# Performance work log

Hardware: AMD Instinct MI355X
Metric: run time of the kernel (lower is better)

Reference implementation:

```python
import jax, jax.numpy as jnp
import numpy as np

BS, EMB, RES = 256, 768, 14
N_MASKS, HID, OUT, N_PROJ = 16, 4096, 256, 4
BN_EPS = 1e-5


def setup_inputs() -> dict:
    key = jax.random.key(0)
    ks = jax.random.split(key, 8)
    x = jax.random.normal(ks[0], (BS, EMB, RES, RES), jnp.float32)
    # binary ROI masks over the 14x14 = 196 patch grid
    masks = (jax.random.uniform(ks[1], (BS, N_MASKS, RES * RES)) < 0.3).astype(jnp.float32)
    projection_idx = jax.random.randint(ks[2], (N_MASKS,), 0, N_PROJ, jnp.int32)
    mask_ids = jax.random.randint(ks[3], (BS, N_MASKS), 0, 100, jnp.int32)
    # stacked params for the N_PROJ MLP projectors
    W1 = jax.random.normal(ks[4], (N_PROJ, EMB, HID), jnp.float32) * 0.02
    b1 = jnp.zeros((N_PROJ, HID), jnp.float32)
    gamma = jnp.ones((N_PROJ, HID), jnp.float32)
    beta = jnp.zeros((N_PROJ, HID), jnp.float32)
    W2 = jax.random.normal(ks[5], (N_PROJ, HID, OUT), jnp.float32) * 0.02
    b2 = jnp.zeros((N_PROJ, OUT), jnp.float32)
    return {"x": x, "masks": masks, "projection_idx": projection_idx,
            "mask_ids": mask_ids, "W1": W1, "b1": b1, "gamma": gamma,
            "beta": beta, "W2": W2, "b2": b2}


def reference(x, masks, projection_idx, mask_ids, W1, b1, gamma, beta, W2, b2):
    bs, emb, hx, hy = x.shape
    # [bs, emb, hx, hy] -> [bs, hw, emb]
    emb_local = jnp.transpose(x, (0, 2, 3, 1)).reshape(bs, hx * hy, emb)
    # mask-normalized pooling:  pooled[b,n,:] = mean of embeddings inside mask n
    area = masks.sum(axis=-1, keepdims=True)
    smpl = masks / jnp.maximum(area, 1.0)
    pooled = smpl @ emb_local                       # [bs, n_masks, emb]
    # dense dispatch: run EVERY projector over all pooled tokens (as original)
    h = jnp.einsum('bne,peh->pbnh', pooled, W1) + b1[:, None, None, :]
    # BatchNorm1d in training mode over flattened (bs*n_masks) batch, per projector
    mu = h.mean(axis=(1, 2), keepdims=True)
    var = jnp.mean(jnp.square(h - mu), axis=(1, 2), keepdims=True)  # biased var
    h = (h - mu) * jax.lax.rsqrt(var + BN_EPS) * gamma[:, None, None, :] + beta[:, None, None, :]
    h = jax.nn.relu(h)
    o = jnp.einsum('pbnh,pho->pbno', h, W2) + b2[:, None, None, :]   # [P, bs, n, out]
    # keep only projector projection_idx[n] for mask-slot n (disjoint selection)
    n_proj = W1.shape[0]
    sel = (projection_idx[None, :] == jnp.arange(n_proj)[:, None]).astype(o.dtype)  # [P, n]
    xs = (o * sel[:, None, :, None]).sum(axis=0)     # [bs, n_masks, out]
    return (xs, mask_ids)
```

## Files before the change

kernel.cpp:

```cpp
#include <hip/hip_runtime.h>
#include <hip/hip_bf16.h>

#define BS 256
#define EMB 768
#define HW 196
#define NMASK 16
#define HID 4096
#define OUT 256
#define NPROJ 4
#define MROWS 4096

typedef __attribute__((ext_vector_type(8))) short bf16x8;
typedef __attribute__((ext_vector_type(4))) float f32x4;
typedef __attribute__((ext_vector_type(8))) unsigned short u16x8;

__device__ inline float bf2f(unsigned short u) {
    unsigned int x = ((unsigned int)u) << 16;
    return __builtin_bit_cast(float, x);
}
__device__ inline short f2bfs(float f) {
    return __builtin_bit_cast(short, __float2bfloat16(f));
}

#define GL16(gptr, lptr)                                                     \
    __builtin_amdgcn_global_load_lds(                                        \
        (const __attribute__((address_space(1))) void*)(gptr),               \
        (__attribute__((address_space(3))) void*)(lptr), 16, 0, 0)

__global__ __launch_bounds__(256) void pool_mfma(
    const float* __restrict__ x, const float* __restrict__ masks,
    __hip_bfloat16* __restrict__ pooledG)
{
    __shared__ __align__(16) short afr[7 * 64 * 8];
    __shared__ float inv[NMASK];
    const int ec = blockIdx.x, b = blockIdx.y, tid = threadIdx.x;
    const float* mb = masks + (size_t)b * NMASK * HW;

    for (int s = tid; s < 7 * 64; s += 256) {
        int m = s & 15, kb = ((s >> 4) & 3) * 8 + (s >> 6) * 32;
        short v[8];
        #pragma unroll
        for (int j = 0; j < 8; ++j) {
            int kk = kb + j;
            v[j] = (kk < HW) ? f2bfs(mb[m * HW + kk]) : (short)0;
        }
        #pragma unroll
        for (int j = 0; j < 8; ++j) afr[s * 8 + j] = v[j];
    }
    if (tid >= 192) {
        int l = tid - 192, m = l >> 2, q = l & 3;
        float a = 0.f;
        for (int hw = q; hw < HW; hw += 4) a += mb[m * HW + hw];
        a += __shfl_xor(a, 1);
        a += __shfl_xor(a, 2);
        if (q == 0) inv[m] = 1.0f / fmaxf(a, 1.0f);
    }
    __syncthreads();

    const int lane = tid & 63, w = tid >> 6;
    const int lc = lane & 15, l4 = lane >> 4;
    const int ebase = ec * 192 + w * 48;
    const bf16x8* afv = (const bf16x8*)afr;
    f32x4 acc[3] = {};

    const float* xb0 = x + ((size_t)b * EMB + ebase + lc) * HW;

    for (int kc = 0; kc < 6; ++kc) {
        bf16x8 af = afv[kc * 64 + lane];
        float4 u[3][2];
        #pragma unroll
        for (int t = 0; t < 3; ++t) {
            const float* xr = xb0 + (size_t)(t * 16) * HW + kc * 32 + l4 * 8;
            u[t][0] = *(const float4*)(xr);
            u[t][1] = *(const float4*)(xr + 4);
        }
        #pragma unroll
        for (int t = 0; t < 3; ++t) {
            bf16x8 bf;
            bf[0] = f2bfs(u[t][0].x); bf[1] = f2bfs(u[t][0].y);
            bf[2] = f2bfs(u[t][0].z); bf[3] = f2bfs(u[t][0].w);
            bf[4] = f2bfs(u[t][1].x); bf[5] = f2bfs(u[t][1].y);
            bf[6] = f2bfs(u[t][1].z); bf[7] = f2bfs(u[t][1].w);
            acc[t] = __builtin_amdgcn_mfma_f32_16x16x32_bf16(af, bf, acc[t], 0, 0, 0);
        }
    }
    {
        bf16x8 af = afv[6 * 64 + lane];
        #pragma unroll
        for (int t = 0; t < 3; ++t) {
            bf16x8 bf = {};
            if (l4 == 0) {
                float4 u0 = *(const float4*)(xb0 + (size_t)(t * 16) * HW + 192);
                bf[0] = f2bfs(u0.x); bf[1] = f2bfs(u0.y);
                bf[2] = f2bfs(u0.z); bf[3] = f2bfs(u0.w);
            }
            acc[t] = __builtin_amdgcn_mfma_f32_16x16x32_bf16(af, bf, acc[t], 0, 0, 0);
        }
    }

    #pragma unroll
    for (int t = 0; t < 3; ++t) {
        int e = ebase + t * 16 + lc;
        #pragma unroll
        for (int j = 0; j < 4; ++j) {
            int m = l4 * 4 + j;
            pooledG[((size_t)m * 256 + b) * EMB + e] =
                __float2bfloat16(acc[t][j] * inv[m]);
        }
    }
}

__global__ __launch_bounds__(256) void transpose_cvt(
    const float* __restrict__ src, __hip_bfloat16* __restrict__ dst, int R, int C)
{
    __shared__ float tile[64][65];
    const float* s = src + (size_t)blockIdx.z * R * C;
    __hip_bfloat16* d = dst + (size_t)blockIdx.z * R * C;
    const int c0 = blockIdx.x * 64, r0 = blockIdx.y * 64, tid = threadIdx.x;
    for (int i = tid; i < 4096; i += 256) {
        int r = i >> 6, c = i & 63;
        tile[r][c] = s[(size_t)(r0 + r) * C + c0 + c];
    }
    __syncthreads();
    for (int i = tid; i < 4096; i += 256) {
        int c = i >> 6, r = i & 63;
        d[(size_t)(c0 + c) * R + r0 + r] = __float2bfloat16(tile[r][c]);
    }
}

__global__ __launch_bounds__(256) void transpose_pg(
    const __hip_bfloat16* __restrict__ src, __hip_bfloat16* __restrict__ dst)
{
    __shared__ __hip_bfloat16 tile[64][65];
    const int c0 = blockIdx.x * 64, r0 = blockIdx.y * 64, tid = threadIdx.x;
    for (int i = tid; i < 4096; i += 256) {
        int r = i >> 6, c = i & 63;
        tile[r][c] = src[(size_t)(r0 + r) * EMB + c0 + c];
    }
    __syncthreads();
    for (int i = tid; i < 4096; i += 256) {
        int c = i >> 6, r = i & 63;
        dst[(size_t)(c0 + c) * MROWS + r0 + r] = tile[r][c];
    }
}

__global__ __launch_bounds__(256) void meanpool(
    const __hip_bfloat16* __restrict__ PT, float* __restrict__ mp)
{
    const int e = blockIdx.x, tid = threadIdx.x;
    const u16x8* p = (const u16x8*)(PT + (size_t)e * MROWS);
    u16x8 v1 = p[tid], v2 = p[tid + 256];
    float s = 0.f;
    #pragma unroll
    for (int j = 0; j < 8; ++j) s += bf2f((unsigned short)v1[j]) + bf2f((unsigned short)v2[j]);
    #pragma unroll
    for (int o = 1; o < 64; o <<= 1) s += __shfl_xor(s, o);
    __shared__ float wsum[4];
    if ((tid & 63) == 0) wsum[tid >> 6] = s;
    __syncthreads();
    if (tid == 0) mp[e] = (wsum[0] + wsum[1] + wsum[2] + wsum[3]) * (1.0f / 4096.0f);
}

__global__ __launch_bounds__(256) void cgemm(
    const __hip_bfloat16* __restrict__ PT, float* __restrict__ Cpart)
{
    __shared__ __align__(16) __hip_bfloat16 As[128 * 32];
    __shared__ __align__(16) __hip_bfloat16 Bs[128 * 32];
    const int tid = threadIdx.x, lane = tid & 63, wid = tid >> 6;
    const int n0 = blockIdx.x * 128, m0 = blockIdx.y * 128, kbase = blockIdx.z * 512;
    float* Cp = Cpart + (size_t)blockIdx.z * EMB * EMB;
    const int wr = wid >> 1, wc = wid & 1;
    const int l4 = lane >> 4, lc = lane & 15;

    f32x4 acc[4][4] = {};
    for (int k0 = kbase; k0 < kbase + 512; k0 += 32) {
        __syncthreads();
        #pragma unroll
        for (int r = 0; r < 2; ++r) {
            int t = r * 256 + tid;
            int row = t >> 2, ko = (t & 3) * 8;
            GL16(PT + (size_t)(m0 + row) * MROWS + k0 + ko, &As[(r * 256 + wid * 64) * 8]);
        }
        #pragma unroll
        for (int r = 0; r < 2; ++r) {
            int t = r * 256 + tid;
            int row = t >> 2, ko = (t & 3) * 8;
            GL16(PT + (size_t)(n0 + row) * MROWS + k0 + ko, &Bs[(r * 256 + wid * 64) * 8]);
        }
        __syncthreads();
        const bf16x8* Av = (const bf16x8*)As;
        const bf16x8* Bv = (const bf16x8*)Bs;
        bf16x8 a[4], b[4];
        #pragma unroll
        for (int m = 0; m < 4; ++m) a[m] = Av[(wr * 64 + m * 16 + lc) * 4 + l4];
        #pragma unroll
        for (int n = 0; n < 4; ++n) b[n] = Bv[(wc * 64 + n * 16 + lc) * 4 + l4];
        #pragma unroll
        for (int m = 0; m < 4; ++m)
            #pragma unroll
            for (int n = 0; n < 4; ++n)
                acc[m][n] = __builtin_amdgcn_mfma_f32_16x16x32_bf16(a[m], b[n], acc[m][n], 0, 0, 0);
    }
    #pragma unroll
    for (int m = 0; m < 4; ++m)
        #pragma unroll
        for (int n = 0; n < 4; ++n)
            #pragma unroll
            for (int j = 0; j < 4; ++j) {
                int row = m0 + wr * 64 + m * 16 + l4 * 4 + j;
                int col = n0 + wc * 64 + n * 16 + lc;
                Cp[(size_t)row * EMB + col] = acc[m][n][j];
            }
}

__global__ __launch_bounds__(256) void cvt_c(
    const float* __restrict__ Cpart, __hip_bfloat16* __restrict__ Cbf)
{
    int i = (blockIdx.x * 256 + threadIdx.x) * 4;
    float sx = 0.f, sy = 0.f, sz = 0.f, sw = 0.f;
    #pragma unroll
    for (int kz = 0; kz < 8; ++kz) {
        float4 v = *(const float4*)(Cpart + (size_t)kz * EMB * EMB + i);
        sx += v.x; sy += v.y; sz += v.z; sw += v.w;
    }
    const float s = 1.0f / 4096.0f;
    Cbf[i + 0] = __float2bfloat16(sx * s);
    Cbf[i + 1] = __float2bfloat16(sy * s);
    Cbf[i + 2] = __float2bfloat16(sz * s);
    Cbf[i + 3] = __float2bfloat16(sw * s);
}

__global__ __launch_bounds__(256) void ugemm(
    const __hip_bfloat16* __restrict__ W1T, const __hip_bfloat16* __restrict__ Cbf,
    const float* __restrict__ mp,
    float* __restrict__ Eh2p, float* __restrict__ Mup)
{
    __shared__ __align__(16) __hip_bfloat16 As[128 * 32];
    __shared__ __align__(16) __hip_bfloat16 Bs[128 * 32];
    const int tid = threadIdx.x, lane = tid & 63, wid = tid >> 6;
    const int n0 = blockIdx.x * 128, m0 = blockIdx.y * 128, p = blockIdx.z;
    const __hip_bfloat16* Ap = W1T + (size_t)p * HID * EMB;
    const int wr = wid >> 1, wc = wid & 1;
    const int l4 = lane >> 4, lc = lane & 15;

    f32x4 acc[4][4] = {};
    for (int k0 = 0; k0 < EMB; k0 += 32) {
        __syncthreads();
        #pragma unroll
        for (int r = 0; r < 2; ++r) {
            int t = r * 256 + tid;
            int row = t >> 2, ko = (t & 3) * 8;
            GL16(Ap + (size_t)(m0 + row) * EMB + k0 + ko, &As[(r * 256 + wid * 64) * 8]);
        }
        #pragma unroll
        for (int r = 0; r < 2; ++r) {
            int t = r * 256 + tid;
            int row = t >> 2, ko = (t & 3) * 8;
            GL16(Cbf + (size_t)(n0 + row) * EMB + k0 + ko, &Bs[(r * 256 + wid * 64) * 8]);
        }
        __syncthreads();
        const bf16x8* Av = (const bf16x8*)As;
        const bf16x8* Bv = (const bf16x8*)Bs;
        bf16x8 a[4], b[4];
        #pragma unroll
        for (int m = 0; m < 4; ++m) a[m] = Av[(wr * 64 + m * 16 + lc) * 4 + l4];
        #pragma unroll
        for (int n = 0; n < 4; ++n) b[n] = Bv[(wc * 64 + n * 16 + lc) * 4 + l4];
        #pragma unroll
        for (int m = 0; m < 4; ++m)
            #pragma unroll
            for (int n = 0; n < 4; ++n)
                acc[m][n] = __builtin_amdgcn_mfma_f32_16x16x32_bf16(a[m], b[n], acc[m][n], 0, 0, 0);
    }

    float mpv[4];
    #pragma unroll
    for (int n = 0; n < 4; ++n) mpv[n] = mp[n0 + wc * 64 + n * 16 + lc];
    #pragma unroll
    for (int m = 0; m < 4; ++m) {
        #pragma unroll
        for (int j = 0; j < 4; ++j) {
            int row = m0 + wr * 64 + m * 16 + l4 * 4 + j;
            const __hip_bfloat16* wrow = Ap + (size_t)row * EMB;
            float e2 = 0.f, mu = 0.f;
            #pragma unroll
            for (int n = 0; n < 4; ++n) {
                int col = n0 + wc * 64 + n * 16 + lc;
                float wv = bf2f(__builtin_bit_cast(unsigned short, wrow[col]));
                e2 += acc[m][n][j] * wv;
                mu += mpv[n] * wv;
            }
            e2 += __shfl_xor(e2, 1); e2 += __shfl_xor(e2, 2);
            e2 += __shfl_xor(e2, 4); e2 += __shfl_xor(e2, 8);
            mu += __shfl_xor(mu, 1); mu += __shfl_xor(mu, 2);
            mu += __shfl_xor(mu, 4); mu += __shfl_xor(mu, 8);
            if (lc == 0) {
                size_t idx = (((size_t)blockIdx.x * 2 + wc) * NPROJ + p) * HID + row;
                Eh2p[idx] = e2;
                Mup [idx] = mu;
            }
        }
    }
}

__global__ __launch_bounds__(256) void finalize(
    const float* __restrict__ Eh2p, const float* __restrict__ Mup,
    const float* __restrict__ gamma, const float* __restrict__ beta,
    float* __restrict__ sbuf, float* __restrict__ tbuf)
{
    int i = blockIdx.x * 256 + threadIdx.x;
    float e2 = 0.f, mu = 0.f;
    #pragma unroll
    for (int bx = 0; bx < 12; ++bx) {
        e2 += Eh2p[bx * (NPROJ * HID) + i];
        mu += Mup [bx * (NPROJ * HID) + i];
    }
    float var = e2 - mu * mu;
    float is  = rsqrtf(fmaxf(var, 0.0f) + 1e-5f);
    float sc  = gamma[i] * is;
    sbuf[i] = sc;
    tbuf[i] = beta[i] - mu * sc;
}

__global__ __launch_bounds__(512, 2) void gemm1_sel(
    const __hip_bfloat16* __restrict__ A, const __hip_bfloat16* __restrict__ W1T,
    const int* __restrict__ proj,
    const float* __restrict__ sbuf, const float* __restrict__ tbuf,
    __hip_bfloat16* __restrict__ hrelu)
{
    __shared__ __align__(16) short LS[2][32768];
    const int tid = threadIdx.x, lane = tid & 63, w = tid >> 6;
    const int wr = w >> 2, wc = w & 3;
    const int lc = lane & 15, l4 = lane >> 4;
    const int n0 = blockIdx.x * 256, m0 = blockIdx.y * 256;
    const int p = proj[blockIdx.y];
    const __hip_bfloat16* Ag = A;
    const __hip_bfloat16* Bg = W1T + (size_t)p * HID * EMB;
    const bf16x8* LSv = (const bf16x8*)LS;

    const int st_row_l = lane >> 3;
    const int st_cs    = lane & 7;
    auto STAGE = [&](int sbf, int t) {
        #pragma unroll
        for (int ab = 0; ab < 2; ++ab) {
            const __hip_bfloat16* g = ab ? Bg : Ag;
            const int rbase = ab ? n0 : m0;
            #pragma unroll
            for (int i = 0; i < 4; ++i) {
                int row = w * 32 + i * 8 + st_row_l;
                int csl = st_cs ^ (row & 7);
                const __hip_bfloat16* src =
                    g + (size_t)(rbase + row) * EMB + t * 64 + csl * 8;
                char* dst = (char*)LS + ab * 32768 + sbf * 65536 + w * 4096 + i * 1024;
                GL16(src, dst);
            }
        }
    };

    f32x4 acc[8][4] = {};

    STAGE(0, 0);
    asm volatile("s_waitcnt vmcnt(0)" ::: "memory");
    __builtin_amdgcn_s_barrier();

    for (int t = 0; t < 12; ++t) {
        const int buf = t & 1;
        if (t + 1 < 12) STAGE(buf ^ 1, t + 1);

        const int vbA = buf * 4096;
        const int vbB = buf * 4096 + 2048;

        bf16x8 bfr[4][2];
        #pragma unroll
        for (int nf = 0; nf < 4; ++nf) {
            int row_b = wc * 64 + nf * 16 + lc;
            #pragma unroll
            for (int ks = 0; ks < 2; ++ks)
                bfr[nf][ks] = LSv[vbB + row_b * 8 + ((ks * 4 + l4) ^ (row_b & 7))];
        }
        #pragma unroll
        for (int q = 0; q < 4; ++q) {
            bf16x8 afr[2][2];
            #pragma unroll
            for (int mf2 = 0; mf2 < 2; ++mf2) {
                int row_a = wr * 128 + (q * 2 + mf2) * 16 + lc;
                #pragma unroll
                for (int ks = 0; ks < 2; ++ks)
                    afr[mf2][ks] = LSv[vbA + row_a * 8 + ((ks * 4 + l4) ^ (row_a & 7))];
            }
            __builtin_amdgcn_s_setprio(1);
            #pragma unroll
            for (int mf2 = 0; mf2 < 2; ++mf2)
                #pragma unroll
                for (int nf = 0; nf < 4; ++nf)
                    #pragma unroll
                    for (int ks = 0; ks < 2; ++ks)
                        acc[q * 2 + mf2][nf] = __builtin_amdgcn_mfma_f32_16x16x32_bf16(
                            afr[mf2][ks], bfr[nf][ks], acc[q * 2 + mf2][nf], 0, 0, 0);
            __builtin_amdgcn_s_setprio(0);
        }

        asm volatile("s_waitcnt vmcnt(0)" ::: "memory");
        __builtin_amdgcn_s_barrier();
    }

    #pragma unroll
    for (int nf = 0; nf < 4; ++nf) {
        int col = n0 + wc * 64 + nf * 16 + lc;
        float s = sbuf[p * HID + col];
        float tt = tbuf[p * HID + col];
        #pragma unroll
        for (int mf = 0; mf < 8; ++mf)
            #pragma unroll
            for (int j = 0; j < 4; ++j) {
                int row = m0 + wr * 128 + mf * 16 + l4 * 4 + j;
                float v = fmaxf(acc[mf][nf][j] * s + tt, 0.0f);
                hrelu[(size_t)row * HID + col] = __float2bfloat16(v);
            }
    }
}

__global__ __launch_bounds__(256) void gemm2(
    const __hip_bfloat16* __restrict__ Hn, const __hip_bfloat16* __restrict__ W2T,
    const int* __restrict__ proj, float* __restrict__ Opart)
{
    __shared__ __align__(16) __hip_bfloat16 As[128 * 32];
    __shared__ __align__(16) __hip_bfloat16 Bs[128 * 32];
    const int tid = threadIdx.x, lane = tid & 63, wid = tid >> 6;
    const int nmask = blockIdx.x;
    const int bc    = blockIdx.y;
    const int ct    = blockIdx.z >> 2, kz = blockIdx.z & 3;
    const int p = proj[nmask];
    const __hip_bfloat16* Ap = Hn + (size_t)(nmask * 256 + bc * 128) * HID;
    const __hip_bfloat16* Bp = W2T + ((size_t)p * OUT + ct * 128) * HID;
    float* Op = Opart + (size_t)kz * MROWS * OUT;
    const int wr = wid >> 1, wc = wid & 1;
    const int l4 = lane >> 4, lc = lane & 15;

    f32x4 acc[4][4] = {};
    for (int k0 = kz * 1024; k0 < kz * 1024 + 1024; k0 += 32) {
        __syncthreads();
        #pragma unroll
        for (int r = 0; r < 2; ++r) {
            int t = r * 256 + tid;
            int row = t >> 2, ko = (t & 3) * 8;
            GL16(Ap + (size_t)row * HID + k0 + ko, &As[(r * 256 + wid * 64) * 8]);
        }
        #pragma unroll
        for (int r = 0; r < 2; ++r) {
            int t = r * 256 + tid;
            int row = t >> 2, ko = (t & 3) * 8;
            GL16(Bp + (size_t)row * HID + k0 + ko, &Bs[(r * 256 + wid * 64) * 8]);
        }
        __syncthreads();
        const bf16x8* Av = (const bf16x8*)As;
        const bf16x8* Bv = (const bf16x8*)Bs;
        bf16x8 a[4], b[4];
        #pragma unroll
        for (int m = 0; m < 4; ++m) a[m] = Av[(wr * 64 + m * 16 + lc) * 4 + l4];
        #pragma unroll
        for (int n = 0; n < 4; ++n) b[n] = Bv[(wc * 64 + n * 16 + lc) * 4 + l4];
        #pragma unroll
        for (int m = 0; m < 4; ++m)
            #pragma unroll
            for (int n = 0; n < 4; ++n)
                acc[m][n] = __builtin_amdgcn_mfma_f32_16x16x32_bf16(a[m], b[n], acc[m][n], 0, 0, 0);
    }

    #pragma unroll
    for (int m = 0; m < 4; ++m)
        #pragma unroll
        for (int n = 0; n < 4; ++n)
            #pragma unroll
            for (int j = 0; j < 4; ++j) {
                int bb = bc * 128 + wr * 64 + m * 16 + l4 * 4 + j;
                int oc = ct * 128 + wc * 64 + n * 16 + lc;
                Op[((size_t)bb * NMASK + nmask) * OUT + oc] = acc[m][n][j];
            }
}

__global__ __launch_bounds__(256) void reduce_out(
    const float* __restrict__ Opart, const float* __restrict__ b2,
    const int* __restrict__ proj, const int* __restrict__ mids,
    float* __restrict__ out)
{
    int i = (blockIdx.x * 256 + threadIdx.x) * 4;
    float sx = 0.f, sy = 0.f, sz = 0.f, sw = 0.f;
    #pragma unroll
    for (int kz = 0; kz < 4; ++kz) {
        float4 v = *(const float4*)(Opart + (size_t)kz * MROWS * OUT + i);
        sx += v.x; sy += v.y; sz += v.z; sw += v.w;
    }
    int nm = (i >> 8) & 15;
    int p  = proj[nm];
    float4 bv = *(const float4*)(b2 + p * OUT + (i & 255));
    float4 r;
    r.x = sx + bv.x; r.y = sy + bv.y; r.z = sz + bv.z; r.w = sw + bv.w;
    *(float4*)(out + i) = r;
    if (blockIdx.x < 16) {
        int t = blockIdx.x * 256 + threadIdx.x;
        out[(size_t)MROWS * OUT + t] = (float)mids[t];
    }
}

extern "C" void kernel_launch(void* const* d_in, const int* in_sizes, int n_in,
                              void* d_out, int out_size, void* d_ws, size_t ws_size,
                              hipStream_t stream)
{
    const float* x     = (const float*)d_in[0];
    const float* masks = (const float*)d_in[1];
    const int*   proj  = (const int*)d_in[2];
    const int*   mids  = (const int*)d_in[3];
    const float* W1    = (const float*)d_in[4];
    const float* gamma = (const float*)d_in[6];
    const float* beta  = (const float*)d_in[7];
    const float* W2    = (const float*)d_in[8];
    const float* b2    = (const float*)d_in[9];
    float* out = (float*)d_out;

    char* ws = (char*)d_ws;
    __hip_bfloat16* pooledG = (__hip_bfloat16*)(ws);
    __hip_bfloat16* W1T     = (__hip_bfloat16*)(ws + 6291456);
    __hip_bfloat16* W2T     = (__hip_bfloat16*)(ws + 31457280);
    float*          mp      = (float*)(ws + 39845888);
    float*          Eh2p    = (float*)(ws + 39848960);
    float*          Mup     = (float*)(ws + 40635392);
    float*          sbuf    = (float*)(ws + 41421824);
    float*          tbuf    = (float*)(ws + 41487360);
    char* R = ws + 41552896;
    __hip_bfloat16* pooledT = (__hip_bfloat16*)(R);
    float*          Cpart   = (float*)(R + 6291456);
    __hip_bfloat16* Cbf     = (__hip_bfloat16*)(R + 25165824);
    __hip_bfloat16* hrelu   = (__hip_bfloat16*)(R);
    float*          Opart   = (float*)(R + 33554432);

    pool_mfma<<<dim3(4, BS), 256, 0, stream>>>(x, masks, pooledG);
    transpose_cvt<<<dim3(HID / 64, EMB / 64, NPROJ), 256, 0, stream>>>(W1, W1T, EMB, HID);
    transpose_cvt<<<dim3(OUT / 64, HID / 64, NPROJ), 256, 0, stream>>>(W2, W2T, HID, OUT);
    transpose_pg<<<dim3(EMB / 64, MROWS / 64), 256, 0, stream>>>(pooledG, pooledT);
    meanpool<<<EMB, 256, 0, stream>>>(pooledT, mp);
    cgemm<<<dim3(6, 6, 8), 256, 0, stream>>>(pooledT, Cpart);
    cvt_c<<<(EMB * EMB) / 1024, 256, 0, stream>>>(Cpart, Cbf);
    ugemm<<<dim3(6, 32, 4), 256, 0, stream>>>(W1T, Cbf, mp, Eh2p, Mup);
    finalize<<<(NPROJ * HID) / 256, 256, 0, stream>>>(Eh2p, Mup, gamma, beta, sbuf, tbuf);
    gemm1_sel<<<dim3(HID / 256, MROWS / 256), 512, 0, stream>>>(pooledG, W1T, proj, sbuf, tbuf, hrelu);
    gemm2<<<dim3(NMASK, 2, 8), 256, 0, stream>>>(hrelu, W2T, proj, Opart);
    reduce_out<<<(MROWS * OUT) / 1024, 256, 0, stream>>>(Opart, b2, proj, mids, out);
}
```

Before: 204.8 us.

## Merge transpose kernels into one launch and triple-buffer gemm1 with half-size K steps

Measured after the change: 202.5 us. Within noise of the previous version (-1.1%).

```diff
diff --git a/kernel.cpp b/kernel.cpp
--- a/kernel.cpp
+++ b/kernel.cpp
@@ -110,37 +110,47 @@
     }
 }
 
-__global__ __launch_bounds__(256) void transpose_cvt(
-    const float* __restrict__ src, __hip_bfloat16* __restrict__ dst, int R, int C)
-{
-    __shared__ float tile[64][65];
-    const float* s = src + (size_t)blockIdx.z * R * C;
-    __hip_bfloat16* d = dst + (size_t)blockIdx.z * R * C;
-    const int c0 = blockIdx.x * 64, r0 = blockIdx.y * 64, tid = threadIdx.x;
-    for (int i = tid; i < 4096; i += 256) {
-        int r = i >> 6, c = i & 63;
-        tile[r][c] = s[(size_t)(r0 + r) * C + c0 + c];
-    }
-    __syncthreads();
-    for (int i = tid; i < 4096; i += 256) {
-        int c = i >> 6, r = i & 63;
-        d[(size_t)(c0 + c) * R + r0 + r] = __float2bfloat16(tile[r][c]);
-    }
-}
-
-__global__ __launch_bounds__(256) void transpose_pg(
-    const __hip_bfloat16* __restrict__ src, __hip_bfloat16* __restrict__ dst)
-{
-    __shared__ __hip_bfloat16 tile[64][65];
-    const int c0 = blockIdx.x * 64, r0 = blockIdx.y * 64, tid = threadIdx.x;
-    for (int i = tid; i < 4096; i += 256) {
-        int r = i >> 6, c = i & 63;
-        tile[r][c] = src[(size_t)(r0 + r) * EMB + c0 + c];
-    }
-    __syncthreads();
-    for (int i = tid; i < 4096; i += 256) {
-        int c = i >> 6, r = i & 63;
-        dst[(size_t)(c0 + c) * MROWS + r0 + r] = tile[r][c];
+__global__ __launch_bounds__(256) void prep(
+    const float* __restrict__ W1, const float* __restrict__ W2,
+    const __hip_bfloat16* __restrict__ pg,
+    __hip_bfloat16* __restrict__ W1T, __hip_bfloat16* __restrict__ W2T,
+    __hip_bfloat16* __restrict__ pgT)
+{
+    __shared__ __align__(16) char sm[64 * 65 * 4];
+    const int bid = blockIdx.x, tid = threadIdx.x;
+    if (bid < 4096) {
+        const float* src; __hip_bfloat16* dst; int R, C, x, y, z;
+        if (bid < 3072) { z = bid / 768; int r = bid % 768; x = r % 64; y = r / 64;
+                          src = W1; dst = W1T; R = EMB; C = HID; }
+        else            { int b2 = bid - 3072; z = b2 / 256; int r = b2 % 256;
+                          x = r % 4; y = r / 4; src = W2; dst = W2T; R = HID; C = OUT; }
+        float (*tile)[65] = (float(*)[65])sm;
+        const float* s = src + (size_t)z * R * C;
+        __hip_bfloat16* d = dst + (size_t)z * R * C;
+        const int c0 = x * 64, r0 = y * 64;
+        for (int i = tid; i < 4096; i += 256) {
+            int r = i >> 6, c = i & 63;
+            tile[r][c] = s[(size_t)(r0 + r) * C + c0 + c];
+        }
+        __syncthreads();
+        for (int i = tid; i < 4096; i += 256) {
+            int c = i >> 6, r = i & 63;
+            d[(size_t)(c0 + c) * R + r0 + r] = __float2bfloat16(tile[r][c]);
+        }
+    } else {
+        const int b3 = bid - 4096;
+        const int x = b3 % 12, y = b3 / 12;
+        __hip_bfloat16 (*tile)[65] = (__hip_bfloat16(*)[65])sm;
+        const int c0 = x * 64, r0 = y * 64;
+        for (int i = tid; i < 4096; i += 256) {
+            int r = i >> 6, c = i & 63;
+            tile[r][c] = pg[(size_t)(r0 + r) * EMB + c0 + c];
+        }
+        __syncthreads();
+        for (int i = tid; i < 4096; i += 256) {
+            int c = i >> 6, r = i & 63;
+            pgT[(size_t)(c0 + c) * MROWS + r0 + r] = tile[r][c];
+        }
     }
 }
 
@@ -328,7 +338,7 @@
     const float* __restrict__ sbuf, const float* __restrict__ tbuf,
     __hip_bfloat16* __restrict__ hrelu)
 {
-    __shared__ __align__(16) short LS[2][32768];
+    __shared__ __align__(16) short LS[3 * 16384];
     const int tid = threadIdx.x, lane = tid & 63, w = tid >> 6;
     const int wr = w >> 2, wc = w & 3;
     const int lc = lane & 15, l4 = lane >> 4;
@@ -338,70 +348,66 @@
     const __hip_bfloat16* Bg = W1T + (size_t)p * HID * EMB;
     const bf16x8* LSv = (const bf16x8*)LS;
 
-    const int st_row_l = lane >> 3;
-    const int st_cs    = lane & 7;
-    auto STAGE = [&](int sbf, int t) {
+    auto STAGE = [&](int t) {
+        const int sb = (t % 3) * 32768;
         #pragma unroll
         for (int ab = 0; ab < 2; ++ab) {
             const __hip_bfloat16* g = ab ? Bg : Ag;
             const int rbase = ab ? n0 : m0;
             #pragma unroll
-            for (int i = 0; i < 4; ++i) {
-                int row = w * 32 + i * 8 + st_row_l;
-                int csl = st_cs ^ (row & 7);
+            for (int i = 0; i < 2; ++i) {
+                int c = (w * 2 + i) * 64 + lane;
+                int row = c >> 2, ps = c & 3;
+                int ls = ps ^ (row & 3);
                 const __hip_bfloat16* src =
-                    g + (size_t)(rbase + row) * EMB + t * 64 + csl * 8;
-                char* dst = (char*)LS + ab * 32768 + sbf * 65536 + w * 4096 + i * 1024;
-                GL16(src, dst);
+                    g + (size_t)(rbase + row) * EMB + t * 32 + ls * 8;
+                GL16(src, (char*)LS + sb + ab * 16384 + (w * 2 + i) * 1024);
             }
         }
     };
 
     f32x4 acc[8][4] = {};
 
-    STAGE(0, 0);
-    asm volatile("s_waitcnt vmcnt(0)" ::: "memory");
+    STAGE(0);
+    STAGE(1);
+    asm volatile("s_waitcnt vmcnt(4)" ::: "memory");
     __builtin_amdgcn_s_barrier();
 
-    for (int t = 0; t < 12; ++t) {
-        const int buf = t & 1;
-        if (t + 1 < 12) STAGE(buf ^ 1, t + 1);
-
-        const int vbA = buf * 4096;
-        const int vbB = buf * 4096 + 2048;
-
-        bf16x8 bfr[4][2];
+    for (int t = 0; t < 24; ++t) {
+        if (t + 2 < 24) STAGE(t + 2);
+        const int vb = (t % 3) * 2048;
+
+        bf16x8 bfr[4];
         #pragma unroll
         for (int nf = 0; nf < 4; ++nf) {
-            int row_b = wc * 64 + nf * 16 + lc;
-            #pragma unroll
-            for (int ks = 0; ks < 2; ++ks)
-                bfr[nf][ks] = LSv[vbB + row_b * 8 + ((ks * 4 + l4) ^ (row_b & 7))];
+            int rb = wc * 64 + nf * 16 + lc;
+            bfr[nf] = LSv[vb + 1024 + rb * 4 + (l4 ^ (rb & 3))];
         }
         #pragma unroll
         for (int q = 0; q < 4; ++q) {
-            bf16x8 afr[2][2];
-            #pragma unroll
-            for (int mf2 = 0; mf2 < 2; ++mf2) {
-                int row_a = wr * 128 + (q * 2 + mf2) * 16 + lc;
-                #pragma unroll
-                for (int ks = 0; ks < 2; ++ks)
-                    afr[mf2][ks] = LSv[vbA + row_a * 8 + ((ks * 4 + l4) ^ (row_a & 7))];
+            bf16x8 afr[2];
+            #pragma unroll
+            for (int m2 = 0; m2 < 2; ++m2) {
+                int ra = wr * 128 + (q * 2 + m2) * 16 + lc;
+                afr[m2] = LSv[vb + ra * 4 + (l4 ^ (ra & 3))];
             }
             __builtin_amdgcn_s_setprio(1);
             #pragma unroll
-            for (int mf2 = 0; mf2 < 2; ++mf2)
+            for (int m2 = 0; m2 < 2; ++m2)
                 #pragma unroll
                 for (int nf = 0; nf < 4; ++nf)
-                    #pragma unroll
-                    for (int ks = 0; ks < 2; ++ks)
-                        acc[q * 2 + mf2][nf] = __builtin_amdgcn_mfma_f32_16x16x32_bf16(
-                            afr[mf2][ks], bfr[nf][ks], acc[q * 2 + mf2][nf], 0, 0, 0);
+                    acc[q * 2 + m2][nf] = __builtin_amdgcn_mfma_f32_16x16x32_bf16(
+                        afr[m2], bfr[nf], acc[q * 2 + m2][nf], 0, 0, 0);
             __builtin_amdgcn_s_setprio(0);
         }
 
-        asm volatile("s_waitcnt vmcnt(0)" ::: "memory");
-        __builtin_amdgcn_s_barrier();
+        if (t + 2 < 24) {
+            asm volatile("s_waitcnt vmcnt(4)" ::: "memory");
+            __builtin_amdgcn_s_barrier();
+        } else if (t + 2 == 24) {
+            asm volatile("s_waitcnt vmcnt(0)" ::: "memory");
+            __builtin_amdgcn_s_barrier();
+        }
     }
 
     #pragma unroll
@@ -535,9 +541,7 @@
     float*          Opart   = (float*)(R + 33554432);
 
     pool_mfma<<<dim3(4, BS), 256, 0, stream>>>(x, masks, pooledG);
-    transpose_cvt<<<dim3(HID / 64, EMB / 64, NPROJ), 256, 0, stream>>>(W1, W1T, EMB, HID);
-    transpose_cvt<<<dim3(OUT / 64, HID / 64, NPROJ), 256, 0, stream>>>(W2, W2T, HID, OUT);
-    transpose_pg<<<dim3(EMB / 64, MROWS / 64), 256, 0, stream>>>(pooledG, pooledT);
+    prep<<<4864, 256, 0, stream>>>(W1, W2, pooledG, W1T, W2T, pooledT);
     meanpool<<<EMB, 256, 0, stream>>>(pooledT, mp);
     cgemm<<<dim3(6, 6, 8), 256, 0, stream>>>(pooledT, Cpart);
     cvt_c<<<(EMB * EMB) / 1024, 256, 0, stream>>>(Cpart, Cbf);
```
